# Kernel optimization log

Hardware: AMD Instinct MI355X
Metric: run time of the kernel (lower is better)

Reference implementation:

```python
import jax, jax.numpy as jnp
import numpy as np

BS, D_HID, D_EMB, N_LABELS = 8192, 1024, 256, 64
EPS = 1e-8  # torch cosine_similarity norm clamp


def _l2norm(x):
    return x / jnp.maximum(jnp.linalg.norm(x, axis=-1, keepdims=True), EPS)


def setup_inputs() -> dict:
    key = jax.random.key(0)
    k1, k2, k3, k4 = jax.random.split(key, 4)
    return {
        "mask_emb": jax.random.normal(k1, (BS, D_HID), dtype=jnp.float32),
        "W": jax.random.normal(k2, (D_EMB, D_HID), dtype=jnp.float32) * 0.02,
        "b": jnp.zeros((D_EMB,), dtype=jnp.float32),
        "label_emb": jax.random.normal(k3, (N_LABELS, D_EMB), dtype=jnp.float32),
        "labels": jax.random.randint(k4, (BS,), 0, N_LABELS, dtype=jnp.int64 if jax.config.jax_enable_x64 else jnp.int32),
    }


def reference(mask_emb, W, b, label_emb, labels):
    bs = mask_emb.shape[0]
    emb = mask_emb @ W.T + b                      # [bs, E] transform_matrix
    en = _l2norm(emb)                              # normalized sample embeddings
    ln = _l2norm(label_emb)                        # normalized prototypes

    S = en @ en.T                                  # [bs, bs] pairwise cosine sim
    C = en @ ln.T                                  # [bs, L]  sample-vs-prototype cosine sim

    same = labels[:, None] == labels[None, :]      # [bs, bs]
    eye = jnp.eye(bs, dtype=bool)
    offdiag = ~eye

    # ---- inter-sample loss ----
    # N[i] = sum over negatives (different label) of exp(S[i,k]); constant over j
    expS = jnp.exp(S)
    N = jnp.sum(jnp.where(~same, expS, 0.0), axis=1)          # [bs]
    # pos_loss is S[i,j] for same-label j!=i, else 0
    P = jnp.where(same & offdiag, S, 0.0)                      # [bs, bs]
    terms = -P + jnp.log(N[:, None] + jnp.exp(P))
    inter = jnp.sum(jnp.where(offdiag, terms, 0.0)) / (bs * bs)

    # ---- sample-prototype losses ----
    pos = jnp.take_along_axis(C, labels[:, None], axis=1)[:, 0]   # C[i, labels[i]]
    onehot = jax.nn.one_hot(labels, label_emb.shape[0], dtype=C.dtype)
    expC = jnp.exp(C)
    neg1 = jnp.sum(expC * (1.0 - onehot), axis=1)                 # sum over other prototypes
    # neg2[i] = sum_{j: labels[j]!=labels[i]} exp(cos(label_emb[labels[i]], emb[j])) = exp(C[j, labels[i]])
    M = expC.T[labels]                                            # [bs, bs], M[i,j] = exp(C[j, labels[i]])
    neg2 = jnp.sum(jnp.where(~same, M, 0.0), axis=1)              # 0 if no negatives -> log(exp(pos)) = pos
    exp_pos = jnp.exp(pos)
    proto1 = jnp.mean(-pos + jnp.log(neg1 + exp_pos))
    proto2 = jnp.mean(-pos + jnp.log(neg2 + exp_pos))

    a1, a2 = 0.5, 0.5
    return a1 * inter + a2 * (proto1 + proto2)
```

## Files before the change

kernel.cpp:

```cpp
#include <hip/hip_runtime.h>
#include <hip/hip_bf16.h>
#include <math.h>

#define BS 8192
#define DH 1024
#define DE 256
#define NL 64
#define SBST 224

typedef __attribute__((ext_vector_type(8))) short short8;
typedef __attribute__((ext_vector_type(4))) float f32x4;
typedef __attribute__((ext_vector_type(4))) int i32x4;
typedef unsigned short ushort;

__device__ __forceinline__ ushort bf16b(float f){
  unsigned u = __float_as_uint(f);
  unsigned r = (u + 0x7FFFu + ((u >> 16) & 1u)) >> 16;
  return (ushort)r;
}

__device__ __forceinline__ float fexp2(float x){
  float r;
  asm("v_exp_f32 %0, %1" : "=v"(r) : "v"(x));
  return r;
}

__device__ __forceinline__ void gload_lds16(const void* g, void* l){
  __builtin_amdgcn_global_load_lds((const __attribute__((address_space(1))) void*)g,
                                   (__attribute__((address_space(3))) void*)l, 16, 0, 0);
}

__global__ __launch_bounds__(256) void prep_kernel(const float* __restrict__ W, ushort* __restrict__ Wb,
    const float* __restrict__ label_emb, ushort* __restrict__ lnb,
    const int* __restrict__ labels, int* __restrict__ cnt,
    int* __restrict__ offs, int* __restrict__ groups){
  int b = blockIdx.x, t = threadIdx.x;
  if (b < 128){
    int i = (b*256 + t) * 8;
    float4 v0 = *(const float4*)(W+i);
    float4 v1 = *(const float4*)(W+i+4);
    short8 o;
    o[0]=bf16b(v0.x); o[1]=bf16b(v0.y); o[2]=bf16b(v0.z); o[3]=bf16b(v0.w);
    o[4]=bf16b(v1.x); o[5]=bf16b(v1.y); o[6]=bf16b(v1.z); o[7]=bf16b(v1.w);
    *(short8*)(Wb+i) = o;
    return;
  }
  if (b < 192){
    __shared__ float red[256];
    int l = b - 128;
    float v = label_emb[l*DE + t];
    red[t] = v*v;
    __syncthreads();
    for (int s=128;s>0;s>>=1){
      if (t<s) red[t] += red[t+s];
      __syncthreads();
    }
    float inv = 1.0f / fmaxf(sqrtf(red[0]), 1e-8f);
    lnb[l*DE + t] = bf16b(v * inv);
    return;
  }
  __shared__ ushort loc[256][64];
  __shared__ int off_s[65];
  __shared__ int cnt_s[64];
  #pragma unroll
  for (int l=0;l<64;l++) loc[t][l]=0;
  __syncthreads();
  int base = t * 32;
  for (int i=0;i<32;i++){
    int y = labels[base+i];
    loc[t][y] = (ushort)(loc[t][y] + 1);
  }
  __syncthreads();
  if (t < 64){
    int run = 0;
    for (int tt=0;tt<256;tt++){
      int v = loc[tt][t];
      loc[tt][t] = (ushort)run;
      run += v;
    }
    cnt_s[t] = run;
    cnt[t] = run;
  }
  __syncthreads();
  if (t == 0){
    int acc = 0;
    for (int l=0;l<64;l++){ off_s[l] = acc; acc += cnt_s[l]; }
    off_s[64] = acc;
  }
  __syncthreads();
  if (t < 65) offs[t] = off_s[t];
  for (int i=0;i<32;i++){
    int idx = base + i;
    int y = labels[idx];
    int p = off_s[y] + loc[t][y];
    loc[t][y] = (ushort)(loc[t][y] + 1);
    groups[p] = idx;
  }
}

#define EMB_LOADA(KB) do { \
  if (tid < 256){ \
    va0 = *(const float4*)(aptr + (KB)); \
    va1 = *(const float4*)(aptr + (KB) + 4); \
  } \
} while(0)

#define EMB_WRITEA(P) do { \
  if (tid < 256){ \
    short8 o; \
    o[0]=bf16b(va0.x); o[1]=bf16b(va0.y); o[2]=bf16b(va0.z); o[3]=bf16b(va0.w); \
    o[4]=bf16b(va1.x); o[5]=bf16b(va1.y); o[6]=bf16b(va1.z); o[7]=bf16b(va1.w); \
    *(short8*)&Ab[P][tid*8] = o; \
  } \
} while(0)

#define EMB_STAGEB(P, KB) do { \
  _Pragma("unroll") \
  for (int q=0;q<4;q++){ \
    int chunk = q*8 + w; \
    int lin = chunk*64 + lane; \
    int row = lin >> 3, cc = lin & 7; \
    int lc = cc ^ (row & 7); \
    gload_lds16(Wb + (size_t)row*DH + (KB) + lc*8, Bb[P] + chunk*512); \
  } \
} while(0)

#define EMB_COMPUTE(P) do { \
  _Pragma("unroll") \
  for (int kk=0;kk<2;kk++){ \
    short8 af[2], bfr[2]; \
    _Pragma("unroll") \
    for (int m=0;m<2;m++){ \
      int row = m*16 + c15; \
      int phys = (kk*4 + qr) ^ (row & 7); \
      af[m] = *(const short8*)&Ab[P][row*64 + phys*8]; \
    } \
    _Pragma("unroll") \
    for (int n=0;n<2;n++){ \
      int row = w*32 + n*16 + c15; \
      int phys = (kk*4 + qr) ^ (row & 7); \
      bfr[n] = *(const short8*)&Bb[P][row*64 + phys*8]; \
    } \
    _Pragma("unroll") \
    for (int m=0;m<2;m++) \
      _Pragma("unroll") \
      for (int n=0;n<2;n++) \
        acc[m][n] = __builtin_amdgcn_mfma_f32_16x16x32_bf16(af[m], bfr[n], acc[m][n], 0,0,0); \
  } \
} while(0)

__global__ __launch_bounds__(512) void emb_kernel(const float* __restrict__ mask,
    const ushort* __restrict__ Wb, const float* __restrict__ bias,
    ushort* __restrict__ enb, signed char* __restrict__ eni8){
  __shared__ ushort Ab[2][32*64];
  __shared__ ushort Bb[2][256*64];
  __shared__ float sq[8][32];
  __shared__ float inv_s[32];
  int tid = threadIdx.x, lane = tid & 63, w = tid >> 6;
  int qr = lane >> 4, c15 = lane & 15;
  int rb = blockIdx.x * 32;
  int arow = tid >> 3, alc = (tid & 7) ^ (arow & 7);
  const float* aptr = mask + (size_t)(rb + (arow & 31))*DH + alc*8;
  float4 va0, va1;
  f32x4 acc[2][2] = {};
  EMB_LOADA(0);
  EMB_WRITEA(0);
  EMB_STAGEB(0, 0);
  __syncthreads();
  int buf = 0;
  for (int kb = 0; kb < 16; kb++){
    if (kb < 15){
      EMB_LOADA((kb+1)*64);
      EMB_STAGEB(buf^1, (kb+1)*64);
    }
    EMB_COMPUTE(buf);
    if (kb < 15) EMB_WRITEA(buf^1);
    __syncthreads();
    buf ^= 1;
  }
  float bv[2];
  #pragma unroll
  for (int n=0;n<2;n++) bv[n] = bias[w*32 + n*16 + c15];
  #pragma unroll
  for (int m=0;m<2;m++){
    #pragma unroll
    for (int r=0;r<4;r++){
      float s = 0.f;
      #pragma unroll
      for (int n=0;n<2;n++){
        float v = acc[m][n][r] + bv[n];
        acc[m][n][r] = v;
        s += v*v;
      }
      #pragma unroll
      for (int msk=8; msk>=1; msk>>=1) s += __shfl_xor(s, msk);
      if (c15 == 0) sq[w][m*16 + qr*4 + r] = s;
    }
  }
  __syncthreads();
  if (tid < 32){
    float s = 0.f;
    #pragma unroll
    for (int q=0;q<8;q++) s += sq[q][tid];
    inv_s[tid] = 1.0f / fmaxf(sqrtf(s), 1e-8f);
  }
  __syncthreads();
  #pragma unroll
  for (int m=0;m<2;m++){
    #pragma unroll
    for (int r=0;r<4;r++){
      int row = m*16 + qr*4 + r;
      float iv = inv_s[row];
      #pragma unroll
      for (int n=0;n<2;n++){
        int col = w*32 + n*16 + c15;
        float v = acc[m][n][r] * iv;
        enb [(size_t)(rb+row)*DE + col] = bf16b(v);
        int q8 = __float2int_rn(v * 127.0f);
        q8 = q8 > 127 ? 127 : (q8 < -127 ? -127 : q8);
        eni8[(size_t)(rb+row)*DE + col] = (signed char)q8;
      }
    }
  }
}

__global__ __launch_bounds__(256, 4) void fused3_kernel(const ushort* __restrict__ enb,
    const signed char* __restrict__ eni8, const ushort* __restrict__ lnb,
    const int* __restrict__ labels, const int* __restrict__ cnt,
    const int* __restrict__ offs, const int* __restrict__ groups,
    float* __restrict__ N_part, float* __restrict__ pos, float* __restrict__ rowsum,
    float* __restrict__ T_part, float* __restrict__ G_part,
    float* __restrict__ samesum, ushort* __restrict__ Sbuf){
  __shared__ __align__(16) char pool[33792];
  int blk = blockIdx.x;
  int tid = threadIdx.x, lane = tid & 63, w = tid >> 6;
  int qr = lane >> 4, c15 = lane & 15;

  if (blk < 128){
    ushort* Ab = (ushort*)pool;
    ushort* Bb = (ushort*)(pool + 8192);
    float* TpS = (float*)(pool + 16384);
    float* GpS = (float*)(pool + 17408);
    int rb = blk * 64;
    f32x4 acc[4] = {};
    for (int kb = 0; kb < DE; kb += 64){
      #pragma unroll
      for (int q=0;q<2;q++){
        int chunk = q*4 + w;
        int lin = chunk*64 + lane;
        int row = lin >> 3, cc = lin & 7;
        int lc = cc ^ (row & 7);
        gload_lds16(enb + (size_t)(rb+row)*DE + kb + lc*8, Ab + chunk*512);
      }
      #pragma unroll
      for (int q=0;q<2;q++){
        int chunk = q*4 + w;
        int lin = chunk*64 + lane;
        int row = lin >> 3, cc = lin & 7;
        int lc = cc ^ (row & 7);
        gload_lds16(lnb + (size_t)row*DE + kb + lc*8, Bb + chunk*512);
      }
      __syncthreads();
      #pragma unroll
      for (int kk=0;kk<2;kk++){
        int arow = w*16 + c15;
        int aphys = (kk*4 + (lane >> 4)) ^ (arow & 7);
        short8 af = *(const short8*)&Ab[arow*64 + aphys*8];
        #pragma unroll
        for (int ni=0;ni<4;ni++){
          int brow = ni*16 + c15;
          int bphys = (kk*4 + (lane >> 4)) ^ (brow & 7);
          short8 bfr = *(const short8*)&Bb[brow*64 + bphys*8];
          acc[ni] = __builtin_amdgcn_mfma_f32_16x16x32_bf16(af, bfr, acc[ni], 0,0,0);
        }
      }
      __syncthreads();
    }
    int yr[4];
    #pragma unroll
    for (int r=0;r<4;r++) yr[r] = labels[rb + w*16 + qr*4 + r];
    float e[4][4];
    #pragma unroll
    for (int ni=0;ni<4;ni++)
      #pragma unroll
      for (int r=0;r<4;r++) e[ni][r] = __expf(acc[ni][r]);
    #pragma unroll
    for (int r=0;r<4;r++){
      float rs = e[0][r]+e[1][r]+e[2][r]+e[3][r];
      float ps = 0.f;
      #pragma unroll
      for (int ni=0;ni<4;ni++) if (ni*16 + c15 == yr[r]) ps = acc[ni][r];
      #pragma unroll
      for (int msk=8; msk>=1; msk>>=1){ rs += __shfl_xor(rs, msk); ps += __shfl_xor(ps, msk); }
      if (c15 == 0){
        int grow = rb + w*16 + qr*4 + r;
        rowsum[grow] = rs;
        pos[grow] = ps;
      }
    }
    #pragma unroll
    for (int ni=0;ni<4;ni++){
      int col = ni*16 + c15;
      float t = 0.f, g = 0.f;
      #pragma unroll
      for (int r=0;r<4;r++){
        t += e[ni][r];
        if (col == yr[r]) g += e[ni][r];
      }
      t += __shfl_xor(t, 16); t += __shfl_xor(t, 32);
      g += __shfl_xor(g, 16); g += __shfl_xor(g, 32);
      if (qr == 0){ TpS[w*64 + col] = t; GpS[w*64 + col] = g; }
    }
    __syncthreads();
    if (tid < 64){
      T_part[(size_t)blk*64 + tid] = TpS[tid]+TpS[64+tid]+TpS[128+tid]+TpS[192+tid];
      G_part[(size_t)blk*64 + tid] = GpS[tid]+GpS[64+tid]+GpS[128+tid]+GpS[192+tid];
    }
    return;
  }

  if (blk < 384){
    ushort* Ab = (ushort*)pool;
    ushort* Bb = (ushort*)(pool + 8192);
    int* aidx = (int*)(pool + 24576);
    int* gidx = (int*)(pool + 24832);
    float* Gs = (float*)(pool + 25344);
    int gid = blk - 128;
    int l = gid & 63, rt = gid >> 6;
    int m = cnt[l], off = offs[l];
    ushort* Sl = Sbuf + (size_t)l * SBST * SBST;
    for (int ra = rt*64; ra < m; ra += 256){
      __syncthreads();
      if (tid < 64){ int a = ra + tid; aidx[tid] = groups[off + (a < m ? a : 0)]; }
      float Ga[4] = {0.f,0.f,0.f,0.f};
      for (int cb2 = 0; cb2 < m; cb2 += 128){
        __syncthreads();
        if (tid < 128){ int bb = cb2 + tid; gidx[tid] = groups[off + (bb < m ? bb : 0)]; }
        __syncthreads();
        f32x4 acc[4][2] = {};
        for (int kb = 0; kb < DE; kb += 64){
          #pragma unroll
          for (int q=0;q<2;q++){
            int chunk = q*4 + w;
            int lin = chunk*64 + lane;
            int row = lin >> 3, cc = lin & 7;
            int lc = cc ^ (row & 7);
            gload_lds16(enb + (size_t)aidx[row]*DE + kb + lc*8, Ab + chunk*512);
          }
          #pragma unroll
          for (int q=0;q<4;q++){
            int chunk = q*4 + w;
            int lin = chunk*64 + lane;
            int row = lin >> 3, cc = lin & 7;
            int lc = cc ^ (row & 7);
            gload_lds16(enb + (size_t)gidx[row]*DE + kb + lc*8, Bb + chunk*512);
          }
          __syncthreads();
          #pragma unroll
          for (int kk=0;kk<2;kk++){
            short8 af[4], bfr[2];
            #pragma unroll
            for (int mi=0;mi<4;mi++){
              int row = mi*16 + c15;
              int phys = (kk*4 + (lane >> 4)) ^ (row & 7);
              af[mi] = *(const short8*)&Ab[row*64 + phys*8];
            }
            #pragma unroll
            for (int ni=0;ni<2;ni++){
              int row = w*32 + ni*16 + c15;
              int phys = (kk*4 + (lane >> 4)) ^ (row & 7);
              bfr[ni] = *(const short8*)&Bb[row*64 + phys*8];
            }
            #pragma unroll
            for (int mi=0;mi<4;mi++)
              #pragma unroll
              for (int ni=0;ni<2;ni++)
                acc[mi][ni] = __builtin_amdgcn_mfma_f32_16x16x32_bf16(bfr[ni], af[mi], acc[mi][ni], 0,0,0);
          }
          __syncthreads();
        }
        #pragma unroll
        for (int mi=0;mi<4;mi++){
          int a = ra + mi*16 + c15;
          bool aok = (a < m);
          #pragma unroll
          for (int ni=0;ni<2;ni++){
            int b0 = cb2 + w*32 + ni*16 + qr*4;
            #pragma unroll
            for (int r=0;r<4;r++){
              int bb = b0 + r;
              float sv = acc[mi][ni][r];
              if (bb < m){
                Ga[mi] += __expf(sv);
                if (aok) Sl[(size_t)a*SBST + bb] = bf16b(sv);
              }
            }
          }
        }
      }
      #pragma unroll
      for (int mi=0;mi<4;mi++){
        float g = Ga[mi];
        g += __shfl_xor(g, 16);
        g += __shfl_xor(g, 32);
        if (lane < 16) Gs[w*64 + mi*16 + lane] = g;
      }
      __syncthreads();
      if (tid < 64 && ra + tid < m)
        samesum[aidx[tid]] = Gs[tid] + Gs[64+tid] + Gs[128+tid] + Gs[192+tid];
    }
    return;
  }

  signed char* Ai = (signed char*)pool;
  signed char* Bi = (signed char*)(pool + 16384);
  float* nred = (float*)(pool + 32768);
  int lin0 = blk - 384;
  int sw = (lin0 & 7) * 512 + (lin0 >> 3);
  int bx = sw & 63, by = sw >> 6;
  int wr = w >> 1, wc = w & 1;
  int rb = bx * 128;
  int cb = by * 128;
  i32x4 acc[4][4] = {};
  for (int kb = 0; kb < 256; kb += 128){
    #pragma unroll
    for (int q=0;q<4;q++){
      int chunk = q*4 + w;
      int lin2 = chunk*64 + lane;
      int row = lin2 >> 3, cc = lin2 & 7;
      int lc = cc ^ (row & 7);
      gload_lds16(eni8 + (size_t)(rb + row)*DE + kb + lc*16, Ai + chunk*1024);
      gload_lds16(eni8 + (size_t)(cb + row)*DE + kb + lc*16, Bi + chunk*1024);
    }
    __syncthreads();
    __builtin_amdgcn_s_setprio(1);
    #pragma unroll
    for (int kk=0;kk<2;kk++){
      i32x4 af[4], bfr[4];
      #pragma unroll
      for (int m=0;m<4;m++){
        int row = wr*64 + m*16 + c15;
        int phys = (kk*4 + qr) ^ (row & 7);
        af[m] = *(const i32x4*)&Ai[row*128 + phys*16];
      }
      #pragma unroll
      for (int n=0;n<4;n++){
        int row = wc*64 + n*16 + c15;
        int phys = (kk*4 + qr) ^ (row & 7);
        bfr[n] = *(const i32x4*)&Bi[row*128 + phys*16];
      }
      #pragma unroll
      for (int m=0;m<4;m++)
        #pragma unroll
        for (int n=0;n<4;n++)
          acc[m][n] = __builtin_amdgcn_mfma_i32_16x16x64_i8(bfr[n], af[m], acc[m][n], 0,0,0);
    }
    __builtin_amdgcn_s_setprio(0);
    __syncthreads();
  }
  const float SC = 1.44269504f / 16129.0f;
  #pragma unroll
  for (int m=0;m<4;m++){
    float s = 0.f;
    #pragma unroll
    for (int n=0;n<4;n++)
      #pragma unroll
      for (int r=0;r<4;r++)
        s += fexp2((float)acc[m][n][r] * SC);
    s += __shfl_xor(s, 16);
    s += __shfl_xor(s, 32);
    if (lane < 16) nred[wc*128 + wr*64 + m*16 + lane] = s;
  }
  __syncthreads();
  if (tid < 128)
    N_part[(size_t)by * BS + rb + tid] = nred[tid] + nred[128 + tid];
}

__global__ __launch_bounds__(256) void tail_kernel(const int* __restrict__ cnt,
    const int* __restrict__ offs, const int* __restrict__ groups,
    const float* __restrict__ N_part, const float* __restrict__ samesum,
    float* __restrict__ Nrow, const ushort* __restrict__ Sbuf,
    float* __restrict__ pairp){
  __shared__ float red[256];
  __shared__ float NaS[32];
  int b = blockIdx.x, tid = threadIdx.x;
  if (b < 32){
    int i = b*256 + tid;
    float s = 0.f;
    #pragma unroll
    for (int c=0;c<64;c++) s += N_part[(size_t)c*BS + i];
    Nrow[i] = s - samesum[i];
    return;
  }
  int pid = b - 32;
  int l = pid & 63, split = pid >> 6;
  int m = cnt[l], off = offs[l];
  const ushort* Sl = Sbuf + (size_t)l * SBST * SBST;
  int r = tid >> 3, c = tid & 7;
  int a = split*32 + r;
  {
    float s0 = 0.f;
    if (a < m){
      int g = groups[off + a];
      #pragma unroll
      for (int q=0;q<8;q++) s0 += N_part[(size_t)(c + q*8)*BS + g];
    }
    #pragma unroll
    for (int msk=4; msk>=1; msk>>=1) s0 += __shfl_xor(s0, msk);
    if (c == 0 && a < m) NaS[r] = s0 - samesum[groups[off + a]];
  }
  __syncthreads();
  float sum = 0.f;
  if (a < m){
    float Na = NaS[r];
    const ushort* Srow = Sl + (size_t)a * SBST;
    int nseg = (m + 7) >> 3;
    for (int st = c; st < nseg; st += 8){
      short8 v = *(const short8*)(Srow + st*8);
      #pragma unroll
      for (int j=0;j<8;j++){
        int b2 = st*8 + j;
        if (b2 < m && b2 != a){
          float s = __uint_as_float((unsigned)(ushort)v[j] << 16);
          sum += -s + __logf(Na + __expf(s));
        }
      }
    }
  }
  red[tid] = sum;
  __syncthreads();
  for (int s=128;s>0;s>>=1){ if (tid<s) red[tid]+=red[tid+s]; __syncthreads(); }
  if (tid==0) pairp[pid] = red[0];
}

__global__ void finalize_kernel(const int* __restrict__ labels, const int* __restrict__ cnt,
    const float* __restrict__ Nrow, const float* __restrict__ pos,
    const float* __restrict__ rowsum, const float* __restrict__ T_part,
    const float* __restrict__ G_part, const float* __restrict__ pairp,
    float* __restrict__ out){
  __shared__ double red[3*256];
  __shared__ float TGp[4][64];
  __shared__ float TGf[64];
  int t = threadIdx.x;
  {
    int l = t & 63, qq = t >> 6;
    float ts = 0.f, gs = 0.f;
    for (int b=qq; b<128; b+=4){ ts += T_part[b*64 + l]; gs += G_part[b*64 + l]; }
    TGp[qq][l] = ts - gs;
  }
  __syncthreads();
  if (t < 64) TGf[t] = TGp[0][t]+TGp[1][t]+TGp[2][t]+TGp[3][t];
  __syncthreads();
  double a=0.0, p1=0.0, p2=0.0;
  for (int i=t; i<BS; i+=256){
    int y = labels[i];
    float Ni = Nrow[i];
    a += (double)((float)(BS - cnt[y]) * __logf(Ni + 1.0f));
    float ps = pos[i];
    p1 += (double)(-ps + __logf(rowsum[i]));
    p2 += (double)(-ps + __logf(TGf[y] + __expf(ps)));
  }
  red[t]=a; red[256+t]=p1; red[512+t]=p2;
  __syncthreads();
  for (int s=128;s>0;s>>=1){
    if (t<s){ red[t]+=red[t+s]; red[256+t]+=red[256+t+s]; red[512+t]+=red[512+t+s]; }
    __syncthreads();
  }
  if (t==0){
    double pair = 0.0;
    for (int l=0;l<512;l++) pair += (double)pairp[l];
    double inter = (red[0] + pair) / ((double)BS * (double)BS);
    double proto = (red[256] + red[512]) / (double)BS;
    out[0] = (float)(0.5*inter + 0.5*proto);
  }
}

extern "C" void kernel_launch(void* const* d_in, const int* in_sizes, int n_in,
                              void* d_out, int out_size, void* d_ws, size_t ws_size,
                              hipStream_t stream){
  const float* mask  = (const float*)d_in[0];
  const float* W     = (const float*)d_in[1];
  const float* bias  = (const float*)d_in[2];
  const float* lemb  = (const float*)d_in[3];
  const int*   labels= (const int*)d_in[4];
  float* out = (float*)d_out;

  ushort* enb    = (ushort*)d_ws;
  signed char* eni8 = (signed char*)(enb + (size_t)BS*DE);
  ushort* Wb     = (ushort*)(eni8 + (size_t)BS*DE);
  ushort* lnb    = Wb + (size_t)DE*DH;
  ushort* Sbuf   = lnb + (size_t)NL*DE;
  float*  N_part = (float*)(Sbuf + (size_t)NL*SBST*SBST);
  float*  Nrow   = N_part + (size_t)64*BS;
  float*  pos    = Nrow + BS;
  float*  rowsum = pos + BS;
  float*  samesum= rowsum + BS;
  float*  T_part = samesum + BS;
  float*  G_part = T_part + 128*64;
  float*  pairp  = G_part + 128*64;
  int* cnt    = (int*)(pairp + 512);
  int* offs   = cnt + NL;
  int* groups = offs + 68;

  hipLaunchKernelGGL(prep_kernel,     dim3(193), dim3(256), 0, stream, W, Wb, lemb, lnb, labels, cnt, offs, groups);
  hipLaunchKernelGGL(emb_kernel,      dim3(BS/32), dim3(512), 0, stream, mask, Wb, bias, enb, eni8);
  hipLaunchKernelGGL(fused3_kernel,   dim3(4480), dim3(256), 0, stream,
                     enb, eni8, lnb, labels, cnt, offs, groups,
                     N_part, pos, rowsum, T_part, G_part, samesum, Sbuf);
  hipLaunchKernelGGL(tail_kernel,     dim3(544), dim3(256), 0, stream,
                     cnt, offs, groups, N_part, samesum, Nrow, Sbuf, pairp);
  hipLaunchKernelGGL(finalize_kernel, dim3(1), dim3(256), 0, stream,
                     labels, cnt, Nrow, pos, rowsum, T_part, G_part, pairp, out);
}
```

Measured before the change: 120.1 us.

## Fold finalize into tail kernel via last-block atomic and spread A-tile loads

Measured after the change: 153.4 us. 27.7% more time.

```diff
diff --git a/kernel.cpp b/kernel.cpp
--- a/kernel.cpp
+++ b/kernel.cpp
@@ -9,6 +9,7 @@
 #define SBST 224
 
 typedef __attribute__((ext_vector_type(8))) short short8;
+typedef __attribute__((ext_vector_type(4))) short short4v;
 typedef __attribute__((ext_vector_type(4))) float f32x4;
 typedef __attribute__((ext_vector_type(4))) int i32x4;
 typedef unsigned short ushort;
@@ -33,7 +34,7 @@
 __global__ __launch_bounds__(256) void prep_kernel(const float* __restrict__ W, ushort* __restrict__ Wb,
     const float* __restrict__ label_emb, ushort* __restrict__ lnb,
     const int* __restrict__ labels, int* __restrict__ cnt,
-    int* __restrict__ offs, int* __restrict__ groups){
+    int* __restrict__ offs, int* __restrict__ groups, int* __restrict__ done){
   int b = blockIdx.x, t = threadIdx.x;
   if (b < 128){
     int i = (b*256 + t) * 8;
@@ -59,6 +60,7 @@
     lnb[l*DE + t] = bf16b(v * inv);
     return;
   }
+  if (t == 0) done[0] = 0;
   __shared__ ushort loc[256][64];
   __shared__ int off_s[65];
   __shared__ int cnt_s[64];
@@ -99,19 +101,13 @@
 }
 
 #define EMB_LOADA(KB) do { \
-  if (tid < 256){ \
-    va0 = *(const float4*)(aptr + (KB)); \
-    va1 = *(const float4*)(aptr + (KB) + 4); \
-  } \
+  va = *(const float4*)(aptr + (KB)); \
 } while(0)
 
 #define EMB_WRITEA(P) do { \
-  if (tid < 256){ \
-    short8 o; \
-    o[0]=bf16b(va0.x); o[1]=bf16b(va0.y); o[2]=bf16b(va0.z); o[3]=bf16b(va0.w); \
-    o[4]=bf16b(va1.x); o[5]=bf16b(va1.y); o[6]=bf16b(va1.z); o[7]=bf16b(va1.w); \
-    *(short8*)&Ab[P][tid*8] = o; \
-  } \
+  short4v o; \
+  o[0]=bf16b(va.x); o[1]=bf16b(va.y); o[2]=bf16b(va.z); o[3]=bf16b(va.w); \
+  *(short4v*)&Ab[P][awr] = o; \
 } while(0)
 
 #define EMB_STAGEB(P, KB) do { \
@@ -159,9 +155,10 @@
   int tid = threadIdx.x, lane = tid & 63, w = tid >> 6;
   int qr = lane >> 4, c15 = lane & 15;
   int rb = blockIdx.x * 32;
-  int arow = tid >> 3, alc = (tid & 7) ^ (arow & 7);
-  const float* aptr = mask + (size_t)(rb + (arow & 31))*DH + alc*8;
-  float4 va0, va1;
+  int arow = tid >> 4, c4 = tid & 15;
+  int awr = arow*64 + (((c4>>1) ^ (arow & 7))*8) + (c4 & 1)*4;
+  const float* aptr = mask + (size_t)(rb + arow)*DH + c4*4;
+  float4 va;
   f32x4 acc[2][2] = {};
   EMB_LOADA(0);
   EMB_WRITEA(0);
@@ -476,13 +473,17 @@
     N_part[(size_t)by * BS + rb + tid] = nred[tid] + nred[128 + tid];
 }
 
-__global__ __launch_bounds__(256) void tail_kernel(const int* __restrict__ cnt,
-    const int* __restrict__ offs, const int* __restrict__ groups,
-    const float* __restrict__ N_part, const float* __restrict__ samesum,
-    float* __restrict__ Nrow, const ushort* __restrict__ Sbuf,
-    float* __restrict__ pairp){
+__global__ __launch_bounds__(256) void tail_kernel(const int* __restrict__ labels,
+    const int* __restrict__ cnt, const int* __restrict__ offs,
+    const int* __restrict__ groups, const float* __restrict__ N_part,
+    const float* __restrict__ samesum, float* __restrict__ Nrow,
+    const ushort* __restrict__ Sbuf, float* __restrict__ pairp,
+    const float* __restrict__ pos, const float* __restrict__ rowsum,
+    const float* __restrict__ T_part, const float* __restrict__ G_part,
+    int* __restrict__ done, float* __restrict__ out){
   __shared__ float red[256];
   __shared__ float NaS[32];
+  __shared__ int lastS;
   int b = blockIdx.x, tid = threadIdx.x;
   if (b < 32){
     int i = b*256 + tid;
@@ -490,88 +491,89 @@
     #pragma unroll
     for (int c=0;c<64;c++) s += N_part[(size_t)c*BS + i];
     Nrow[i] = s - samesum[i];
-    return;
-  }
-  int pid = b - 32;
-  int l = pid & 63, split = pid >> 6;
-  int m = cnt[l], off = offs[l];
-  const ushort* Sl = Sbuf + (size_t)l * SBST * SBST;
-  int r = tid >> 3, c = tid & 7;
-  int a = split*32 + r;
+  } else {
+    int pid = b - 32;
+    int l = pid & 63, split = pid >> 6;
+    int m = cnt[l], off = offs[l];
+    const ushort* Sl = Sbuf + (size_t)l * SBST * SBST;
+    int r = tid >> 3, c = tid & 7;
+    int a = split*32 + r;
+    {
+      float s0 = 0.f;
+      if (a < m){
+        int g = groups[off + a];
+        #pragma unroll
+        for (int q=0;q<8;q++) s0 += N_part[(size_t)(c + q*8)*BS + g];
+      }
+      #pragma unroll
+      for (int msk=4; msk>=1; msk>>=1) s0 += __shfl_xor(s0, msk);
+      if (c == 0 && a < m) NaS[r] = s0 - samesum[groups[off + a]];
+    }
+    __syncthreads();
+    float sum = 0.f;
+    if (a < m){
+      float Na = NaS[r];
+      const ushort* Srow = Sl + (size_t)a * SBST;
+      int nseg = (m + 7) >> 3;
+      for (int st = c; st < nseg; st += 8){
+        short8 v = *(const short8*)(Srow + st*8);
+        #pragma unroll
+        for (int j=0;j<8;j++){
+          int b2 = st*8 + j;
+          if (b2 < m && b2 != a){
+            float s = __uint_as_float((unsigned)(ushort)v[j] << 16);
+            sum += -s + __logf(Na + __expf(s));
+          }
+        }
+      }
+    }
+    red[tid] = sum;
+    __syncthreads();
+    for (int s=128;s>0;s>>=1){ if (tid<s) red[tid]+=red[tid+s]; __syncthreads(); }
+    if (tid==0) pairp[pid] = red[0];
+  }
+  __syncthreads();
+  __threadfence();
+  if (tid == 0) lastS = (atomicAdd(done, 1) == 543) ? 1 : 0;
+  __syncthreads();
+  if (!lastS) return;
+  __threadfence();
   {
-    float s0 = 0.f;
-    if (a < m){
-      int g = groups[off + a];
-      #pragma unroll
-      for (int q=0;q<8;q++) s0 += N_part[(size_t)(c + q*8)*BS + g];
-    }
-    #pragma unroll
-    for (int msk=4; msk>=1; msk>>=1) s0 += __shfl_xor(s0, msk);
-    if (c == 0 && a < m) NaS[r] = s0 - samesum[groups[off + a]];
-  }
-  __syncthreads();
-  float sum = 0.f;
-  if (a < m){
-    float Na = NaS[r];
-    const ushort* Srow = Sl + (size_t)a * SBST;
-    int nseg = (m + 7) >> 3;
-    for (int st = c; st < nseg; st += 8){
-      short8 v = *(const short8*)(Srow + st*8);
-      #pragma unroll
-      for (int j=0;j<8;j++){
-        int b2 = st*8 + j;
-        if (b2 < m && b2 != a){
-          float s = __uint_as_float((unsigned)(ushort)v[j] << 16);
-          sum += -s + __logf(Na + __expf(s));
-        }
-      }
-    }
-  }
-  red[tid] = sum;
-  __syncthreads();
-  for (int s=128;s>0;s>>=1){ if (tid<s) red[tid]+=red[tid+s]; __syncthreads(); }
-  if (tid==0) pairp[pid] = red[0];
-}
-
-__global__ void finalize_kernel(const int* __restrict__ labels, const int* __restrict__ cnt,
-    const float* __restrict__ Nrow, const float* __restrict__ pos,
-    const float* __restrict__ rowsum, const float* __restrict__ T_part,
-    const float* __restrict__ G_part, const float* __restrict__ pairp,
-    float* __restrict__ out){
-  __shared__ double red[3*256];
-  __shared__ float TGp[4][64];
-  __shared__ float TGf[64];
-  int t = threadIdx.x;
-  {
-    int l = t & 63, qq = t >> 6;
-    float ts = 0.f, gs = 0.f;
-    for (int b=qq; b<128; b+=4){ ts += T_part[b*64 + l]; gs += G_part[b*64 + l]; }
-    TGp[qq][l] = ts - gs;
-  }
-  __syncthreads();
-  if (t < 64) TGf[t] = TGp[0][t]+TGp[1][t]+TGp[2][t]+TGp[3][t];
-  __syncthreads();
-  double a=0.0, p1=0.0, p2=0.0;
-  for (int i=t; i<BS; i+=256){
-    int y = labels[i];
-    float Ni = Nrow[i];
-    a += (double)((float)(BS - cnt[y]) * __logf(Ni + 1.0f));
-    float ps = pos[i];
-    p1 += (double)(-ps + __logf(rowsum[i]));
-    p2 += (double)(-ps + __logf(TGf[y] + __expf(ps)));
-  }
-  red[t]=a; red[256+t]=p1; red[512+t]=p2;
-  __syncthreads();
-  for (int s=128;s>0;s>>=1){
-    if (t<s){ red[t]+=red[t+s]; red[256+t]+=red[256+t+s]; red[512+t]+=red[512+t+s]; }
-    __syncthreads();
-  }
-  if (t==0){
-    double pair = 0.0;
-    for (int l=0;l<512;l++) pair += (double)pairp[l];
-    double inter = (red[0] + pair) / ((double)BS * (double)BS);
-    double proto = (red[256] + red[512]) / (double)BS;
-    out[0] = (float)(0.5*inter + 0.5*proto);
+    __shared__ double dred[3*256];
+    __shared__ float TGp[4][64];
+    __shared__ float TGf[64];
+    int t = tid;
+    {
+      int l = t & 63, qq = t >> 6;
+      float ts = 0.f, gs = 0.f;
+      for (int bb=qq; bb<128; bb+=4){ ts += T_part[bb*64 + l]; gs += G_part[bb*64 + l]; }
+      TGp[qq][l] = ts - gs;
+    }
+    __syncthreads();
+    if (t < 64) TGf[t] = TGp[0][t]+TGp[1][t]+TGp[2][t]+TGp[3][t];
+    __syncthreads();
+    double a=0.0, p1=0.0, p2=0.0;
+    for (int i=t; i<BS; i+=256){
+      int y = labels[i];
+      float Ni = Nrow[i];
+      a += (double)((float)(BS - cnt[y]) * __logf(Ni + 1.0f));
+      float ps = pos[i];
+      p1 += (double)(-ps + __logf(rowsum[i]));
+      p2 += (double)(-ps + __logf(TGf[y] + __expf(ps)));
+    }
+    dred[t]=a; dred[256+t]=p1; dred[512+t]=p2;
+    __syncthreads();
+    for (int s=128;s>0;s>>=1){
+      if (t<s){ dred[t]+=dred[t+s]; dred[256+t]+=dred[256+t+s]; dred[512+t]+=dred[512+t+s]; }
+      __syncthreads();
+    }
+    if (t==0){
+      double pair = 0.0;
+      for (int l=0;l<512;l++) pair += (double)pairp[l];
+      double inter = (dred[0] + pair) / ((double)BS * (double)BS);
+      double proto = (dred[256] + dred[512]) / (double)BS;
+      out[0] = (float)(0.5*inter + 0.5*proto);
+    }
   }
 }
 
@@ -601,14 +603,14 @@
   int* cnt    = (int*)(pairp + 512);
   int* offs   = cnt + NL;
   int* groups = offs + 68;
-
-  hipLaunchKernelGGL(prep_kernel,     dim3(193), dim3(256), 0, stream, W, Wb, lemb, lnb, labels, cnt, offs, groups);
+  int* done   = groups + BS;
+
+  hipLaunchKernelGGL(prep_kernel,     dim3(193), dim3(256), 0, stream, W, Wb, lemb, lnb, labels, cnt, offs, groups, done);
   hipLaunchKernelGGL(emb_kernel,      dim3(BS/32), dim3(512), 0, stream, mask, Wb, bias, enb, eni8);
   hipLaunchKernelGGL(fused3_kernel,   dim3(4480), dim3(256), 0, stream,
                      enb, eni8, lnb, labels, cnt, offs, groups,
                      N_part, pos, rowsum, T_part, G_part, samesum, Sbuf);
   hipLaunchKernelGGL(tail_kernel,     dim3(544), dim3(256), 0, stream,
-                     cnt, offs, groups, N_part, samesum, Nrow, Sbuf, pairp);
-  hipLaunchKernelGGL(finalize_kernel, dim3(1), dim3(256), 0, stream,
-                     labels, cnt, Nrow, pos, rowsum, T_part, G_part, pairp, out);
-}
+                     labels, cnt, offs, groups, N_part, samesum, Nrow, Sbuf, pairp,
+                     pos, rowsum, T_part, G_part, done, out);
+}
```
